# Optimization experiments

Hardware: AMD Instinct MI355X
Metric: run time of the kernel (lower is better)

Reference implementation:

```python
import jax, jax.numpy as jnp
import numpy as np

D_MODEL, HEADS, D_K = 512, 8, 64
MIN_SPREAD, MIN_RBF, MAX_RBF = 2.0, 0.001, 1.0
NEG_INF = float('-inf')


def setup_inputs() -> dict:
    key = jax.random.key(0)
    ks = jax.random.split(key, 12)
    B, N = 2, 2048
    xav = (6.0 / (D_K + D_MODEL)) ** 0.5
    unif = lambda k, shape: jax.random.uniform(k, shape, jnp.float32, -xav, xav)
    return {
        'q': jax.random.normal(ks[0], (B, N, D_MODEL), jnp.float32),
        'k': jax.random.normal(ks[1], (B, N, D_MODEL), jnp.float32),
        'v': jax.random.normal(ks[2], (B, N, D_MODEL), jnp.float32),
        'coords': jax.random.normal(ks[3], (B, N, 3), jnp.float32),
        'mask': jnp.zeros((B, N), dtype=bool),
        'spread_weights': jnp.zeros((HEADS,), jnp.float32),
        'beta_weights': jnp.zeros((HEADS,), jnp.float32),
        'q_proj': unif(ks[4], (HEADS, D_MODEL, D_K)),
        'k_proj': unif(ks[5], (HEADS, D_MODEL, D_K)),
        'v_proj': unif(ks[6], (HEADS, D_MODEL, D_K)),
        'q_bias': jnp.zeros((HEADS, D_K), jnp.float32),
        'k_bias': jnp.zeros((HEADS, D_K), jnp.float32),
        'v_bias': jnp.zeros((HEADS, D_K), jnp.float32),
        'w_out': jax.random.normal(ks[7], (D_MODEL, D_MODEL), jnp.float32) * (1.0 / D_MODEL ** 0.5),
    }


def reference(q, k, v, coords, mask, spread_weights, beta_weights,
              q_proj, k_proj, v_proj, q_bias, k_bias, v_bias, w_out):
    B, N, _ = q.shape
    # per-head projections: [B,H,N,dk]
    Q = jnp.einsum('bnd,hdk->bhnk', q, q_proj) + q_bias[None, :, None, :]
    K = jnp.einsum('bnd,hdk->bhnk', k, k_proj) + k_bias[None, :, None, :]
    V = jnp.einsum('bnd,hdk->bhnk', v, v_proj) + v_bias[None, :, None, :]
    # scaled dot-product scores [B,H,N,N]
    S = jnp.einsum('bhnk,bhmk->bhnm', Q, K) / (D_K ** 0.5)
    # squared pairwise distances [B,N,N] (D = sqrt(D2); RBF uses -D^2 = -D2)
    D2 = jnp.sum((coords[:, :, None, :] - coords[:, None, :, :]) ** 2, axis=-1)
    spreads = MIN_SPREAD + jnp.exp(spread_weights)  # [H]
    betas = jnp.exp(beta_weights)                   # [H]
    R = jnp.exp(-D2[:, None, :, :] / (2.0 * spreads[None, :, None, None] ** 2))
    R_norm = 2.0 * (R - MIN_RBF) / (MAX_RBF - MIN_RBF) - 1.0
    SR = S + jnp.abs(S) * betas[None, :, None, None] * R_norm
    SR = jnp.where(mask[:, None, None, :], NEG_INF, SR)  # eval mode: drop_p = 0
    P = jax.nn.softmax(SR, axis=-1)
    out = jnp.einsum('bhnm,bhmk->bhnk', P, V)  # [B,H,N,dk]
    # permute(0,2,3,1) -> [B,N,dk,H], reshape to [B,N,d_model]
    out = jnp.transpose(out, (0, 2, 3, 1)).reshape(B, N, D_MODEL)
    return out @ w_out.T
```

## Files before the change

### kernel.cpp

```cpp
#include <hip/hip_runtime.h>
#include <hip/hip_fp16.h>

typedef unsigned short u16;
typedef __attribute__((ext_vector_type(4))) float f32x4;
typedef __attribute__((ext_vector_type(8))) short s16x8;

#define NTHREADS 256
#define B_SZ 2
#define N_SZ 2048
#define H_SZ 8
#define DK 64
#define DM 512

static __device__ inline void mfma_f16(f32x4& acc, s16x8 a, s16x8 b) {
    asm volatile("v_mfma_f32_16x16x32_f16 %0, %1, %2, %0" : "+v"(acc) : "v"(a), "v"(b));
}

static __device__ inline u16 f16_rn(float f) {
    __half h = __float2half(f);
    return __half_as_ushort(h);
}

static __device__ inline s16x8 cvt8(const float4& a, const float4& b) {
    s16x8 r;
    r[0] = (short)f16_rn(a.x); r[1] = (short)f16_rn(a.y);
    r[2] = (short)f16_rn(a.z); r[3] = (short)f16_rn(a.w);
    r[4] = (short)f16_rn(b.x); r[5] = (short)f16_rn(b.y);
    r[6] = (short)f16_rn(b.z); r[7] = (short)f16_rn(b.w);
    return r;
}

__global__ void __launch_bounds__(NTHREADS) k_prep_proj(
    const float* __restrict__ qp, const float* __restrict__ kp,
    const float* __restrict__ vp, u16* __restrict__ Pt) {
    int ddt = blockIdx.x, h = blockIdx.y, z = blockIdx.z;
    const float* src = (z == 0 ? qp : (z == 1 ? kp : vp)) + (size_t)h * DM * DK;
    u16* dst = Pt + ((size_t)(z * H_SZ + h)) * DK * DM;
    __shared__ float lds[64 * 65];
    int t = threadIdx.x;
#pragma unroll
    for (int i = 0; i < 16; i++) {
        int idx = i * 256 + t;
        int rr = idx >> 6, cc = idx & 63;
        lds[cc * 65 + rr] = src[(size_t)(ddt * 64 + rr) * DK + cc];
    }
    __syncthreads();
#pragma unroll
    for (int i = 0; i < 16; i++) {
        int idx = i * 256 + t;
        int kk = idx >> 6, dd = idx & 63;
        dst[(size_t)kk * DM + ddt * 64 + dd] = f16_rn(lds[kk * 65 + dd]);
    }
}

__global__ void __launch_bounds__(NTHREADS) k_cvt_wout(
    const float* __restrict__ w, u16* __restrict__ wb) {
    int i = (blockIdx.x * 256 + threadIdx.x) * 4;
    float4 f = *(const float4*)(w + i);
    ushort4 r;
    r.x = f16_rn(f.x); r.y = f16_rn(f.y); r.z = f16_rn(f.z); r.w = f16_rn(f.w);
    *(ushort4*)(wb + i) = r;
}

__global__ void __launch_bounds__(NTHREADS) k_proj_gemm(
    const float* __restrict__ q, const float* __restrict__ k,
    const float* __restrict__ v, const u16* __restrict__ Pt,
    const float* __restrict__ qbias, const float* __restrict__ kbias,
    const float* __restrict__ vbias,
    u16* __restrict__ Qb, u16* __restrict__ Kb, u16* __restrict__ Vt) {
    int z = blockIdx.z;
    const float* A = z == 0 ? q : (z == 1 ? k : v);
    const float* bias = z == 0 ? qbias : (z == 1 ? kbias : vbias);
    const u16* Bw = Pt + (size_t)z * DM * DM;
    int m0 = blockIdx.x * 128, c0 = blockIdx.y * 64;
    int t = threadIdx.x, w = t >> 6, l = t & 63, g = l >> 4, cl = l & 15;
    __shared__ __align__(16) u16 a_lds[128 * 40];
    f32x4 acc[2][4] = {};
    int arow = t >> 1, ahalf = t & 1;
    const float* asrc = A + (size_t)(m0 + arow) * DM + ahalf * 16;
    u16* awr = &a_lds[arow * 40 + ahalf * 16];
    for (int ks = 0; ks < 16; ks++) {
        float4 f0 = *(const float4*)(asrc + ks * 32 + 0);
        float4 f1 = *(const float4*)(asrc + ks * 32 + 4);
        float4 f2 = *(const float4*)(asrc + ks * 32 + 8);
        float4 f3 = *(const float4*)(asrc + ks * 32 + 12);
        s16x8 bfrag[4];
#pragma unroll
        for (int st = 0; st < 4; st++) {
            int c = c0 + st * 16 + cl;
            bfrag[st] = *(const s16x8*)(Bw + (size_t)c * DM + ks * 32 + 8 * g);
        }
        __syncthreads();
        *(s16x8*)(awr) = cvt8(f0, f1);
        *(s16x8*)(awr + 8) = cvt8(f2, f3);
        __syncthreads();
#pragma unroll
        for (int rs = 0; rs < 2; rs++) {
            s16x8 afrag = *(const s16x8*)&a_lds[(w * 32 + rs * 16 + cl) * 40 + 8 * g];
#pragma unroll
            for (int st = 0; st < 4; st++) mfma_f16(acc[rs][st], afrag, bfrag[st]);
        }
    }
#pragma unroll
    for (int rs = 0; rs < 2; rs++) {
#pragma unroll
        for (int st = 0; st < 4; st++) {
            int c = c0 + st * 16 + cl;
            int h = c >> 6, kk = c & 63;
            float bv = bias[c];
#pragma unroll
            for (int r = 0; r < 4; r++) {
                int m = m0 + w * 32 + rs * 16 + 4 * g + r;
                int b = m >> 11, n = m & 2047;
                u16 o = f16_rn(acc[rs][st][r] + bv);
                if (z == 2) {
                    Vt[((size_t)((b * H_SZ + h) * 32 + (n >> 6))) * 4096 + kk * 64 + (n & 63)] = o;
                } else {
                    u16* dst = (z == 0) ? Qb : Kb;
                    dst[((size_t)(b * H_SZ + h) * N_SZ + n) * DK + kk] = o;
                }
            }
        }
    }
}

__global__ void __launch_bounds__(NTHREADS) k_attn(
    const u16* __restrict__ Qb, const u16* __restrict__ Kb,
    const u16* __restrict__ Vt, const float* __restrict__ coords,
    const unsigned char* __restrict__ maskp,
    const float* __restrict__ spread_w, const float* __restrict__ beta_w,
    float* __restrict__ Omat) {
    int qt = blockIdx.x, h = blockIdx.y, b = blockIdx.z;
    int n0 = qt * 64;
    int t = threadIdx.x, w = t >> 6, l = t & 63, g = l >> 4, cl = l & 15;
    int bh = b * H_SZ + h;
    __shared__ __align__(16) u16 k_lds[64 * 72];
    __shared__ __align__(16) u16 v_lds[64 * 72];
    __shared__ __align__(16) u16 p_lds[4][16 * 72];
    __shared__ float cj[64 * 4];
    __shared__ unsigned char msk[64];

    int qrow = n0 + w * 16 + cl;
    const u16* qp = Qb + ((size_t)bh * N_SZ + qrow) * DK;
    s16x8 qf0 = *(const s16x8*)(qp + 8 * g);
    s16x8 qf1 = *(const s16x8*)(qp + 32 + 8 * g);

    float qcx[4], qcy[4], qcz[4];
#pragma unroll
    for (int r = 0; r < 4; r++) {
        int row = n0 + w * 16 + 4 * g + r;
        const float* cp = coords + ((size_t)b * N_SZ + row) * 3;
        qcx[r] = cp[0]; qcy[r] = cp[1]; qcz[r] = cp[2];
    }
    float sigma = 2.0f + __expf(spread_w[h]);
    float ninv = -1.0f / (2.0f * sigma * sigma);
    float beta = __expf(beta_w[h]);

    float mrun[4] = {-1e30f, -1e30f, -1e30f, -1e30f};
    float lsum[4] = {0.f, 0.f, 0.f, 0.f};
    f32x4 oacc[4] = {};
    int srow = t >> 2, sq = t & 3;

    for (int jt = 0; jt < 32; jt++) {
        int j0 = jt * 64;
        __syncthreads();
        {
            const u16* ksrc = Kb + ((size_t)bh * N_SZ + j0 + srow) * DK + sq * 16;
            *(s16x8*)&k_lds[srow * 72 + sq * 16 + 0] = *(const s16x8*)(ksrc);
            *(s16x8*)&k_lds[srow * 72 + sq * 16 + 8] = *(const s16x8*)(ksrc + 8);
            const u16* vsrc = Vt + ((size_t)(bh * 32 + jt)) * 4096 + srow * 64 + sq * 16;
            *(s16x8*)&v_lds[srow * 72 + sq * 16 + 0] = *(const s16x8*)(vsrc);
            *(s16x8*)&v_lds[srow * 72 + sq * 16 + 8] = *(const s16x8*)(vsrc + 8);
            if (t < 64) {
                const float* cp = coords + ((size_t)b * N_SZ + j0 + t) * 3;
                cj[t * 4] = cp[0]; cj[t * 4 + 1] = cp[1]; cj[t * 4 + 2] = cp[2];
                msk[t] = maskp[b * N_SZ + j0 + t];
            }
        }
        __syncthreads();

        f32x4 s[4];
#pragma unroll
        for (int st = 0; st < 4; st++) {
            int jj = st * 16 + cl;
            s16x8 kf0 = *(const s16x8*)&k_lds[jj * 72 + 8 * g];
            s16x8 kf1 = *(const s16x8*)&k_lds[jj * 72 + 32 + 8 * g];
            f32x4 a = {};
            mfma_f16(a, qf0, kf0);
            mfma_f16(a, qf1, kf1);
            s[st] = a;
        }

        float sr[4][4];
#pragma unroll
        for (int st = 0; st < 4; st++) {
            int jj = st * 16 + cl;
            float cx = cj[jj * 4], cy = cj[jj * 4 + 1], cz = cj[jj * 4 + 2];
            bool mk = msk[jj] != 0;
#pragma unroll
            for (int r = 0; r < 4; r++) {
                float sv = s[st][r] * 0.125f;
                float dx = qcx[r] - cx, dy = qcy[r] - cy, dz = qcz[r] - cz;
                float d2 = dx * dx + dy * dy + dz * dz;
                float rb = __expf(d2 * ninv);
                float rn = fmaf(2.002002f, rb, -1.002002f);
                sv = fmaf(fabsf(sv) * beta, rn, sv);
                sr[st][r] = mk ? -1e30f : sv;
            }
        }
#pragma unroll
        for (int r = 0; r < 4; r++) {
            float tm = fmaxf(fmaxf(sr[0][r], sr[1][r]), fmaxf(sr[2][r], sr[3][r]));
            tm = fmaxf(tm, __shfl_xor(tm, 1));
            tm = fmaxf(tm, __shfl_xor(tm, 2));
            tm = fmaxf(tm, __shfl_xor(tm, 4));
            tm = fmaxf(tm, __shfl_xor(tm, 8));
            float mn = fmaxf(mrun[r], tm);
            float corr = __expf(mrun[r] - mn);
            mrun[r] = mn;
            lsum[r] *= corr;
#pragma unroll
            for (int dst = 0; dst < 4; dst++) oacc[dst][r] *= corr;
        }
#pragma unroll
        for (int st = 0; st < 4; st++) {
#pragma unroll
            for (int r = 0; r < 4; r++) {
                float p = __expf(sr[st][r] - mrun[r]);
                lsum[r] += p;
                p_lds[w][(4 * g + r) * 72 + st * 16 + cl] = f16_rn(p);
            }
        }
#pragma unroll
        for (int kstep = 0; kstep < 2; kstep++) {
            s16x8 pf = *(const s16x8*)&p_lds[w][cl * 72 + kstep * 32 + 8 * g];
#pragma unroll
            for (int dst = 0; dst < 4; dst++) {
                s16x8 vf = *(const s16x8*)&v_lds[(dst * 16 + cl) * 72 + kstep * 32 + 8 * g];
                mfma_f16(oacc[dst], pf, vf);
            }
        }
    }
#pragma unroll
    for (int r = 0; r < 4; r++) {
        float s = lsum[r];
        s += __shfl_xor(s, 1); s += __shfl_xor(s, 2);
        s += __shfl_xor(s, 4); s += __shfl_xor(s, 8);
        lsum[r] = 1.0f / s;
    }
#pragma unroll
    for (int dst = 0; dst < 4; dst++) {
#pragma unroll
        for (int r = 0; r < 4; r++) {
            int row = n0 + w * 16 + 4 * g + r;
            int col = (dst * 16 + cl) * 8 + h;
            Omat[((size_t)b * N_SZ + row) * DM + col] = oacc[dst][r] * lsum[r];
        }
    }
}

__global__ void __launch_bounds__(NTHREADS) k_out_gemm(
    const float* __restrict__ Omat, const u16* __restrict__ Wb,
    float* __restrict__ out) {
    int m0 = blockIdx.x * 128, c0 = blockIdx.y * 64;
    int t = threadIdx.x, w = t >> 6, l = t & 63, g = l >> 4, cl = l & 15;
    __shared__ __align__(16) u16 a_lds[128 * 40];
    f32x4 acc[2][4] = {};
    int arow = t >> 1, ahalf = t & 1;
    const float* asrc = Omat + (size_t)(m0 + arow) * DM + ahalf * 16;
    u16* awr = &a_lds[arow * 40 + ahalf * 16];
    for (int ks = 0; ks < 16; ks++) {
        float4 f0 = *(const float4*)(asrc + ks * 32 + 0);
        float4 f1 = *(const float4*)(asrc + ks * 32 + 4);
        float4 f2 = *(const float4*)(asrc + ks * 32 + 8);
        float4 f3 = *(const float4*)(asrc + ks * 32 + 12);
        s16x8 bfrag[4];
#pragma unroll
        for (int st = 0; st < 4; st++) {
            int c = c0 + st * 16 + cl;
            bfrag[st] = *(const s16x8*)(Wb + (size_t)c * DM + ks * 32 + 8 * g);
        }
        __syncthreads();
        *(s16x8*)(awr) = cvt8(f0, f1);
        *(s16x8*)(awr + 8) = cvt8(f2, f3);
        __syncthreads();
#pragma unroll
        for (int rs = 0; rs < 2; rs++) {
            s16x8 afrag = *(const s16x8*)&a_lds[(w * 32 + rs * 16 + cl) * 40 + 8 * g];
#pragma unroll
            for (int st = 0; st < 4; st++) mfma_f16(acc[rs][st], afrag, bfrag[st]);
        }
    }
#pragma unroll
    for (int rs = 0; rs < 2; rs++) {
#pragma unroll
        for (int st = 0; st < 4; st++) {
            int c = c0 + st * 16 + cl;
#pragma unroll
            for (int r = 0; r < 4; r++) {
                int m = m0 + w * 32 + rs * 16 + 4 * g + r;
                out[(size_t)m * DM + c] = acc[rs][st][r];
            }
        }
    }
}

extern "C" void kernel_launch(void* const* d_in, const int* in_sizes, int n_in,
                              void* d_out, int out_size, void* d_ws, size_t ws_size,
                              hipStream_t stream) {
    const float* q      = (const float*)d_in[0];
    const float* k      = (const float*)d_in[1];
    const float* v      = (const float*)d_in[2];
    const float* coords = (const float*)d_in[3];
    const unsigned char* mask = (const unsigned char*)d_in[4];
    const float* sw     = (const float*)d_in[5];
    const float* bw     = (const float*)d_in[6];
    const float* qp     = (const float*)d_in[7];
    const float* kp     = (const float*)d_in[8];
    const float* vp     = (const float*)d_in[9];
    const float* qbias  = (const float*)d_in[10];
    const float* kbias  = (const float*)d_in[11];
    const float* vbias  = (const float*)d_in[12];
    const float* wo     = (const float*)d_in[13];

    char* ws = (char*)d_ws;
    u16*   Pt   = (u16*)(ws);
    u16*   Wb   = (u16*)(ws + 1572864);
    u16*   Qb   = (u16*)(ws + 2097152);
    u16*   Kb   = (u16*)(ws + 6291456);
    u16*   Vt   = (u16*)(ws + 10485760);
    float* Omat = (float*)(ws + 14680064);

    k_prep_proj<<<dim3(8, 8, 3), NTHREADS, 0, stream>>>(qp, kp, vp, Pt);
    k_cvt_wout<<<dim3(256), NTHREADS, 0, stream>>>(wo, Wb);
    k_proj_gemm<<<dim3(32, 8, 3), NTHREADS, 0, stream>>>(q, k, v, Pt, qbias, kbias, vbias, Qb, Kb, Vt);
    k_attn<<<dim3(32, 8, 2), NTHREADS, 0, stream>>>(Qb, Kb, Vt, coords, mask, sw, bw, Omat);
    k_out_gemm<<<dim3(32, 8), NTHREADS, 0, stream>>>(Omat, Wb, (float*)d_out);
}
```

Before: 247.4 us.

## Split attention KV across two wave groups, swizzle LDS, precast activations to f16

Merges the prep kernels into one launch and pre-converts q/k/v to f16 so the projection GEMM can stage A tiles with direct global-to-LDS loads into XOR-swizzled shared memory using a larger K step. The attention kernel now runs 512 threads and splits the KV sequence between two wave halves, merging their softmax states at the end. It also folds the 1/sqrt(dk) scale into Q, skips the online-softmax rescale unless the max grows by more than a threshold, and remaps block ids. The output GEMM reads an f16 attention output with smaller tiles. These changes add extra memory traffic for the f16 copy of the inputs and a shared-memory merge step.

New measurement: 215.9 us. -12.7%, faster.

```diff
diff --git a/kernel.cpp b/kernel.cpp
--- a/kernel.cpp
+++ b/kernel.cpp
@@ -5,7 +5,6 @@
 typedef __attribute__((ext_vector_type(4))) float f32x4;
 typedef __attribute__((ext_vector_type(8))) short s16x8;
 
-#define NTHREADS 256
 #define B_SZ 2
 #define N_SZ 2048
 #define H_SZ 8
@@ -15,11 +14,7 @@
 static __device__ inline void mfma_f16(f32x4& acc, s16x8 a, s16x8 b) {
     asm volatile("v_mfma_f32_16x16x32_f16 %0, %1, %2, %0" : "+v"(acc) : "v"(a), "v"(b));
 }
-
-static __device__ inline u16 f16_rn(float f) {
-    __half h = __float2half(f);
-    return __half_as_ushort(h);
-}
+static __device__ inline u16 f16_rn(float f) { return __half_as_ushort(__float2half(f)); }
 
 static __device__ inline s16x8 cvt8(const float4& a, const float4& b) {
     s16x8 r;
@@ -30,77 +25,115 @@
     return r;
 }
 
-__global__ void __launch_bounds__(NTHREADS) k_prep_proj(
-    const float* __restrict__ qp, const float* __restrict__ kp,
-    const float* __restrict__ vp, u16* __restrict__ Pt) {
-    int ddt = blockIdx.x, h = blockIdx.y, z = blockIdx.z;
-    const float* src = (z == 0 ? qp : (z == 1 ? kp : vp)) + (size_t)h * DM * DK;
-    u16* dst = Pt + ((size_t)(z * H_SZ + h)) * DK * DM;
+static __device__ inline u16* swz(u16* base, int row, int byteoff) {
+    return (u16*)((char*)base + row * 128 + (byteoff ^ ((row & 7) << 4)));
+}
+static __device__ inline const u16* swzc(const u16* base, int row, int byteoff) {
+    return (const u16*)((const char*)base + row * 128 + (byteoff ^ ((row & 7) << 4)));
+}
+
+#if __has_builtin(__builtin_amdgcn_global_load_lds)
+#define HAS_GLL 1
+static __device__ inline void gll16(const u16* g, u16* l) {
+    __builtin_amdgcn_global_load_lds(
+        (const __attribute__((address_space(1))) unsigned int*)g,
+        (__attribute__((address_space(3))) unsigned int*)l, 16, 0, 0);
+}
+#endif
+
+static __device__ inline void stage16(const u16* gp, u16* lbase, int lane) {
+#ifdef HAS_GLL
+    gll16(gp, lbase);
+#else
+    *(s16x8*)(lbase + lane * 8) = *(const s16x8*)(gp);
+#endif
+}
+
+__global__ void __launch_bounds__(256) k_prep(
+    const float* __restrict__ q, const float* __restrict__ k,
+    const float* __restrict__ v, const float* __restrict__ qp,
+    const float* __restrict__ kp, const float* __restrict__ vp,
+    const float* __restrict__ wo,
+    u16* __restrict__ Pt, u16* __restrict__ Wb, u16* __restrict__ Af) {
+    int blk = blockIdx.x, t = threadIdx.x;
     __shared__ float lds[64 * 65];
-    int t = threadIdx.x;
-#pragma unroll
-    for (int i = 0; i < 16; i++) {
-        int idx = i * 256 + t;
-        int rr = idx >> 6, cc = idx & 63;
-        lds[cc * 65 + rr] = src[(size_t)(ddt * 64 + rr) * DK + cc];
-    }
-    __syncthreads();
-#pragma unroll
-    for (int i = 0; i < 16; i++) {
-        int idx = i * 256 + t;
-        int kk = idx >> 6, dd = idx & 63;
-        dst[(size_t)kk * DM + ddt * 64 + dd] = f16_rn(lds[kk * 65 + dd]);
-    }
-}
-
-__global__ void __launch_bounds__(NTHREADS) k_cvt_wout(
-    const float* __restrict__ w, u16* __restrict__ wb) {
-    int i = (blockIdx.x * 256 + threadIdx.x) * 4;
-    float4 f = *(const float4*)(w + i);
-    ushort4 r;
-    r.x = f16_rn(f.x); r.y = f16_rn(f.y); r.z = f16_rn(f.z); r.w = f16_rn(f.w);
-    *(ushort4*)(wb + i) = r;
-}
-
-__global__ void __launch_bounds__(NTHREADS) k_proj_gemm(
-    const float* __restrict__ q, const float* __restrict__ k,
-    const float* __restrict__ v, const u16* __restrict__ Pt,
+    if (blk < 192) {
+        int z = blk >> 6, rem = blk & 63, h = rem >> 3, ddt = rem & 7;
+        const float* src = (z == 0 ? qp : (z == 1 ? kp : vp)) + (size_t)h * DM * DK;
+        u16* dst = Pt + ((size_t)(z * H_SZ + h)) * DK * DM;
+#pragma unroll
+        for (int i = 0; i < 16; i++) {
+            int idx = i * 256 + t;
+            int rr = idx >> 6, cc = idx & 63;
+            lds[cc * 65 + rr] = src[(size_t)(ddt * 64 + rr) * DK + cc];
+        }
+        __syncthreads();
+#pragma unroll
+        for (int i = 0; i < 16; i++) {
+            int idx = i * 256 + t;
+            int kk = idx >> 6, dd = idx & 63;
+            dst[(size_t)kk * DM + ddt * 64 + dd] = f16_rn(lds[kk * 65 + dd]);
+        }
+    } else if (blk < 448) {
+        int i = (blk - 192) * 1024 + t * 4;
+        float4 f = *(const float4*)(wo + i);
+        ushort4 r;
+        r.x = f16_rn(f.x); r.y = f16_rn(f.y); r.z = f16_rn(f.z); r.w = f16_rn(f.w);
+        *(ushort4*)(Wb + i) = r;
+    } else {
+        size_t base = (size_t)(blk - 448) * 2048 + (size_t)t * 8;
+        int z = (int)(base >> 21);
+        size_t off = base & 2097151;
+        const float* s = (z == 0 ? q : (z == 1 ? k : v)) + off;
+        float4 f0 = *(const float4*)(s);
+        float4 f1 = *(const float4*)(s + 4);
+        *(s16x8*)(Af + base) = cvt8(f0, f1);
+    }
+}
+
+__global__ void __launch_bounds__(256) k_proj_gemm(
+    const u16* __restrict__ Af, const u16* __restrict__ Pt,
     const float* __restrict__ qbias, const float* __restrict__ kbias,
     const float* __restrict__ vbias,
     u16* __restrict__ Qb, u16* __restrict__ Kb, u16* __restrict__ Vt) {
     int z = blockIdx.z;
-    const float* A = z == 0 ? q : (z == 1 ? k : v);
+    const u16* A = Af + (size_t)z * (4096 * 512);
     const float* bias = z == 0 ? qbias : (z == 1 ? kbias : vbias);
-    const u16* Bw = Pt + (size_t)z * DM * DM;
+    const u16* Bw = Pt + (size_t)z * (512 * 512);
     int m0 = blockIdx.x * 128, c0 = blockIdx.y * 64;
-    int t = threadIdx.x, w = t >> 6, l = t & 63, g = l >> 4, cl = l & 15;
-    __shared__ __align__(16) u16 a_lds[128 * 40];
+    int t = threadIdx.x, w = t >> 6, l = t & 63, g = (l >> 4), cl = l & 15;
+    __shared__ __align__(16) u16 a_lds[128 * 64];
     f32x4 acc[2][4] = {};
-    int arow = t >> 1, ahalf = t & 1;
-    const float* asrc = A + (size_t)(m0 + arow) * DM + ahalf * 16;
-    u16* awr = &a_lds[arow * 40 + ahalf * 16];
-    for (int ks = 0; ks < 16; ks++) {
-        float4 f0 = *(const float4*)(asrc + ks * 32 + 0);
-        float4 f1 = *(const float4*)(asrc + ks * 32 + 4);
-        float4 f2 = *(const float4*)(asrc + ks * 32 + 8);
-        float4 f3 = *(const float4*)(asrc + ks * 32 + 12);
-        s16x8 bfrag[4];
+    int srow_b = w * 8 + (l >> 3), schk = l & 7;
+    for (int ks = 0; ks < 8; ks++) {
+        __syncthreads();
+#pragma unroll
+        for (int cc = 0; cc < 4; cc++) {
+            int row = cc * 32 + srow_b;
+            const u16* gp = A + (size_t)(m0 + row) * 512 + ks * 64 + ((schk ^ (row & 7)) << 3);
+            stage16(gp, a_lds + cc * 2048 + w * 512, l);
+        }
+        s16x8 bfrag[4][2];
 #pragma unroll
         for (int st = 0; st < 4; st++) {
             int c = c0 + st * 16 + cl;
-            bfrag[st] = *(const s16x8*)(Bw + (size_t)c * DM + ks * 32 + 8 * g);
-        }
-        __syncthreads();
-        *(s16x8*)(awr) = cvt8(f0, f1);
-        *(s16x8*)(awr + 8) = cvt8(f2, f3);
+#pragma unroll
+            for (int kk = 0; kk < 2; kk++)
+                bfrag[st][kk] = *(const s16x8*)(Bw + (size_t)c * 512 + ks * 64 + kk * 32 + 8 * g);
+        }
         __syncthreads();
 #pragma unroll
         for (int rs = 0; rs < 2; rs++) {
-            s16x8 afrag = *(const s16x8*)&a_lds[(w * 32 + rs * 16 + cl) * 40 + 8 * g];
-#pragma unroll
-            for (int st = 0; st < 4; st++) mfma_f16(acc[rs][st], afrag, bfrag[st]);
-        }
-    }
+            int row = w * 32 + rs * 16 + cl;
+#pragma unroll
+            for (int kk = 0; kk < 2; kk++) {
+                s16x8 afrag = *(const s16x8*)swzc(a_lds, row, kk * 64 + 16 * g);
+#pragma unroll
+                for (int st = 0; st < 4; st++) mfma_f16(acc[rs][st], afrag, bfrag[st][kk]);
+            }
+        }
+    }
+    float sc = (z == 0) ? 0.125f : 1.0f;
 #pragma unroll
     for (int rs = 0; rs < 2; rs++) {
 #pragma unroll
@@ -112,7 +145,7 @@
             for (int r = 0; r < 4; r++) {
                 int m = m0 + w * 32 + rs * 16 + 4 * g + r;
                 int b = m >> 11, n = m & 2047;
-                u16 o = f16_rn(acc[rs][st][r] + bv);
+                u16 o = f16_rn((acc[rs][st][r] + bv) * sc);
                 if (z == 2) {
                     Vt[((size_t)((b * H_SZ + h) * 32 + (n >> 6))) * 4096 + kk * 64 + (n & 63)] = o;
                 } else {
@@ -124,23 +157,26 @@
     }
 }
 
-__global__ void __launch_bounds__(NTHREADS) k_attn(
+__global__ void __launch_bounds__(512, 4) k_attn(
     const u16* __restrict__ Qb, const u16* __restrict__ Kb,
     const u16* __restrict__ Vt, const float* __restrict__ coords,
     const unsigned char* __restrict__ maskp,
     const float* __restrict__ spread_w, const float* __restrict__ beta_w,
-    float* __restrict__ Omat) {
-    int qt = blockIdx.x, h = blockIdx.y, b = blockIdx.z;
+    u16* __restrict__ Om) {
+    int bid = blockIdx.x;
+    int wid = (bid & 7) * 64 + (bid >> 3);
+    int qt = wid & 31, bh = wid >> 5;
+    int h = bh & 7, b = bh >> 3;
     int n0 = qt * 64;
-    int t = threadIdx.x, w = t >> 6, l = t & 63, g = l >> 4, cl = l & 15;
-    int bh = b * H_SZ + h;
-    __shared__ __align__(16) u16 k_lds[64 * 72];
-    __shared__ __align__(16) u16 v_lds[64 * 72];
-    __shared__ __align__(16) u16 p_lds[4][16 * 72];
-    __shared__ float cj[64 * 4];
-    __shared__ unsigned char msk[64];
-
-    int qrow = n0 + w * 16 + cl;
+    int t = threadIdx.x, w = t >> 6, l = t & 63, g = (l >> 4), cl = l & 15;
+    int wq = w & 3, half = w >> 2;
+    __shared__ __align__(16) u16 kbuf[2][4096];
+    __shared__ __align__(16) u16 vbuf[2][4096];
+    __shared__ __align__(16) u16 pbuf[8][1024];
+    __shared__ float cjs[2][64][4];
+    __shared__ unsigned char msks[2][64];
+
+    int qrow = n0 + wq * 16 + cl;
     const u16* qp = Qb + ((size_t)bh * N_SZ + qrow) * DK;
     s16x8 qf0 = *(const s16x8*)(qp + 8 * g);
     s16x8 qf1 = *(const s16x8*)(qp + 32 + 8 * g);
@@ -148,7 +184,7 @@
     float qcx[4], qcy[4], qcz[4];
 #pragma unroll
     for (int r = 0; r < 4; r++) {
-        int row = n0 + w * 16 + 4 * g + r;
+        int row = n0 + wq * 16 + 4 * g + r;
         const float* cp = coords + ((size_t)b * N_SZ + row) * 3;
         qcx[r] = cp[0]; qcy[r] = cp[1]; qcz[r] = cp[2];
     }
@@ -159,22 +195,26 @@
     float mrun[4] = {-1e30f, -1e30f, -1e30f, -1e30f};
     float lsum[4] = {0.f, 0.f, 0.f, 0.f};
     f32x4 oacc[4] = {};
-    int srow = t >> 2, sq = t & 3;
-
-    for (int jt = 0; jt < 32; jt++) {
-        int j0 = jt * 64;
+    int sid = t & 255, shalf = t >> 8, srow = sid >> 2, sq = sid & 3;
+    const u16* kbase = Kb + (size_t)bh * N_SZ * DK;
+    const u16* vbase = Vt + (size_t)bh * 32 * 4096;
+
+    for (int it = 0; it < 16; it++) {
+        int jts = it * 2 + shalf, j0s = jts * 64;
         __syncthreads();
         {
-            const u16* ksrc = Kb + ((size_t)bh * N_SZ + j0 + srow) * DK + sq * 16;
-            *(s16x8*)&k_lds[srow * 72 + sq * 16 + 0] = *(const s16x8*)(ksrc);
-            *(s16x8*)&k_lds[srow * 72 + sq * 16 + 8] = *(const s16x8*)(ksrc + 8);
-            const u16* vsrc = Vt + ((size_t)(bh * 32 + jt)) * 4096 + srow * 64 + sq * 16;
-            *(s16x8*)&v_lds[srow * 72 + sq * 16 + 0] = *(const s16x8*)(vsrc);
-            *(s16x8*)&v_lds[srow * 72 + sq * 16 + 8] = *(const s16x8*)(vsrc + 8);
-            if (t < 64) {
-                const float* cp = coords + ((size_t)b * N_SZ + j0 + t) * 3;
-                cj[t * 4] = cp[0]; cj[t * 4 + 1] = cp[1]; cj[t * 4 + 2] = cp[2];
-                msk[t] = maskp[b * N_SZ + j0 + t];
+            const u16* ksrc = kbase + (size_t)(j0s + srow) * 64 + sq * 16;
+            *(s16x8*)swz(kbuf[shalf], srow, sq * 32)      = *(const s16x8*)(ksrc);
+            *(s16x8*)swz(kbuf[shalf], srow, sq * 32 + 16) = *(const s16x8*)(ksrc + 8);
+            const u16* vsrc = vbase + (size_t)jts * 4096 + srow * 64 + sq * 16;
+            *(s16x8*)swz(vbuf[shalf], srow, sq * 32)      = *(const s16x8*)(vsrc);
+            *(s16x8*)swz(vbuf[shalf], srow, sq * 32 + 16) = *(const s16x8*)(vsrc + 8);
+            if (sid < 64) {
+                const float* cp = coords + ((size_t)b * N_SZ + j0s + sid) * 3;
+                cjs[shalf][sid][0] = cp[0];
+                cjs[shalf][sid][1] = cp[1];
+                cjs[shalf][sid][2] = cp[2];
+                msks[shalf][sid] = maskp[b * N_SZ + j0s + sid];
             }
         }
         __syncthreads();
@@ -183,31 +223,31 @@
 #pragma unroll
         for (int st = 0; st < 4; st++) {
             int jj = st * 16 + cl;
-            s16x8 kf0 = *(const s16x8*)&k_lds[jj * 72 + 8 * g];
-            s16x8 kf1 = *(const s16x8*)&k_lds[jj * 72 + 32 + 8 * g];
+            s16x8 kf0 = *(const s16x8*)swzc(kbuf[half], jj, 16 * g);
+            s16x8 kf1 = *(const s16x8*)swzc(kbuf[half], jj, 64 + 16 * g);
             f32x4 a = {};
             mfma_f16(a, qf0, kf0);
             mfma_f16(a, qf1, kf1);
             s[st] = a;
         }
-
         float sr[4][4];
 #pragma unroll
         for (int st = 0; st < 4; st++) {
             int jj = st * 16 + cl;
-            float cx = cj[jj * 4], cy = cj[jj * 4 + 1], cz = cj[jj * 4 + 2];
-            bool mk = msk[jj] != 0;
+            float cx = cjs[half][jj][0], cy = cjs[half][jj][1], cz = cjs[half][jj][2];
+            bool mk = msks[half][jj] != 0;
 #pragma unroll
             for (int r = 0; r < 4; r++) {
-                float sv = s[st][r] * 0.125f;
+                float sv = s[st][r];
                 float dx = qcx[r] - cx, dy = qcy[r] - cy, dz = qcz[r] - cz;
-                float d2 = dx * dx + dy * dy + dz * dz;
+                float d2 = fmaf(dx, dx, fmaf(dy, dy, dz * dz));
                 float rb = __expf(d2 * ninv);
                 float rn = fmaf(2.002002f, rb, -1.002002f);
                 sv = fmaf(fabsf(sv) * beta, rn, sv);
                 sr[st][r] = mk ? -1e30f : sv;
             }
         }
+        float tmx[4]; int need = 0;
 #pragma unroll
         for (int r = 0; r < 4; r++) {
             float tm = fmaxf(fmaxf(sr[0][r], sr[1][r]), fmaxf(sr[2][r], sr[3][r]));
@@ -215,12 +255,19 @@
             tm = fmaxf(tm, __shfl_xor(tm, 2));
             tm = fmaxf(tm, __shfl_xor(tm, 4));
             tm = fmaxf(tm, __shfl_xor(tm, 8));
-            float mn = fmaxf(mrun[r], tm);
-            float corr = __expf(mrun[r] - mn);
-            mrun[r] = mn;
-            lsum[r] *= corr;
-#pragma unroll
-            for (int dst = 0; dst < 4; dst++) oacc[dst][r] *= corr;
+            tmx[r] = tm;
+            if (tm > mrun[r] + 8.0f) need = 1;
+        }
+        if (__any(need)) {
+#pragma unroll
+            for (int r = 0; r < 4; r++) {
+                float mn = fmaxf(mrun[r], tmx[r]);
+                float corr = __expf(mrun[r] - mn);
+                mrun[r] = mn;
+                lsum[r] *= corr;
+#pragma unroll
+                for (int dst = 0; dst < 4; dst++) oacc[dst][r] *= corr;
+            }
         }
 #pragma unroll
         for (int st = 0; st < 4; st++) {
@@ -228,15 +275,16 @@
             for (int r = 0; r < 4; r++) {
                 float p = __expf(sr[st][r] - mrun[r]);
                 lsum[r] += p;
-                p_lds[w][(4 * g + r) * 72 + st * 16 + cl] = f16_rn(p);
+                int row = 4 * g + r;
+                *swz(pbuf[w], row, (st * 16 + cl) * 2) = f16_rn(p);
             }
         }
 #pragma unroll
         for (int kstep = 0; kstep < 2; kstep++) {
-            s16x8 pf = *(const s16x8*)&p_lds[w][cl * 72 + kstep * 32 + 8 * g];
+            s16x8 pf = *(const s16x8*)swzc(pbuf[w], cl, kstep * 64 + 16 * g);
 #pragma unroll
             for (int dst = 0; dst < 4; dst++) {
-                s16x8 vf = *(const s16x8*)&v_lds[(dst * 16 + cl) * 72 + kstep * 32 + 8 * g];
+                s16x8 vf = *(const s16x8*)swzc(vbuf[half], dst * 16 + cl, kstep * 64 + 16 * g);
                 mfma_f16(oacc[dst], pf, vf);
             }
         }
@@ -246,61 +294,83 @@
         float s = lsum[r];
         s += __shfl_xor(s, 1); s += __shfl_xor(s, 2);
         s += __shfl_xor(s, 4); s += __shfl_xor(s, 8);
-        lsum[r] = 1.0f / s;
-    }
-#pragma unroll
-    for (int dst = 0; dst < 4; dst++) {
+        lsum[r] = s;
+    }
+    __syncthreads();
+    float* scrO = (float*)(&kbuf[0][0]);
+    float* scrM = (float*)(&vbuf[0][0]);
+    if (half == 1) {
 #pragma unroll
         for (int r = 0; r < 4; r++) {
-            int row = n0 + w * 16 + 4 * g + r;
-            int col = (dst * 16 + cl) * 8 + h;
-            Omat[((size_t)b * N_SZ + row) * DM + col] = oacc[dst][r] * lsum[r];
-        }
-    }
-}
-
-__global__ void __launch_bounds__(NTHREADS) k_out_gemm(
-    const float* __restrict__ Omat, const u16* __restrict__ Wb,
+            int rr = 4 * g + r;
+#pragma unroll
+            for (int dst = 0; dst < 4; dst++)
+                scrO[wq * 1024 + rr * 64 + dst * 16 + cl] = oacc[dst][r];
+            if (cl == 0) {
+                scrM[wq * 32 + rr] = mrun[r];
+                scrM[wq * 32 + 16 + rr] = lsum[r];
+            }
+        }
+    }
+    __syncthreads();
+    if (half == 0) {
+#pragma unroll
+        for (int r = 0; r < 4; r++) {
+            int rr = 4 * g + r;
+            float mu = scrM[wq * 32 + rr], lu = scrM[wq * 32 + 16 + rr];
+            float M = fmaxf(mrun[r], mu);
+            float pa = __expf(mrun[r] - M), pb = __expf(mu - M);
+            float inv = 1.0f / (pa * lsum[r] + pb * lu);
+            int row = n0 + wq * 16 + rr;
+#pragma unroll
+            for (int dst = 0; dst < 4; dst++) {
+                float o = (pa * oacc[dst][r] + pb * scrO[wq * 1024 + rr * 64 + dst * 16 + cl]) * inv;
+                Om[((size_t)b * N_SZ + row) * DM + (dst * 16 + cl) * 8 + h] = f16_rn(o);
+            }
+        }
+    }
+}
+
+__global__ void __launch_bounds__(256) k_out_gemm(
+    const u16* __restrict__ Om, const u16* __restrict__ Wb,
     float* __restrict__ out) {
-    int m0 = blockIdx.x * 128, c0 = blockIdx.y * 64;
-    int t = threadIdx.x, w = t >> 6, l = t & 63, g = l >> 4, cl = l & 15;
-    __shared__ __align__(16) u16 a_lds[128 * 40];
-    f32x4 acc[2][4] = {};
-    int arow = t >> 1, ahalf = t & 1;
-    const float* asrc = Omat + (size_t)(m0 + arow) * DM + ahalf * 16;
-    u16* awr = &a_lds[arow * 40 + ahalf * 16];
-    for (int ks = 0; ks < 16; ks++) {
-        float4 f0 = *(const float4*)(asrc + ks * 32 + 0);
-        float4 f1 = *(const float4*)(asrc + ks * 32 + 4);
-        float4 f2 = *(const float4*)(asrc + ks * 32 + 8);
-        float4 f3 = *(const float4*)(asrc + ks * 32 + 12);
-        s16x8 bfrag[4];
+    int m0 = blockIdx.x * 64, c0 = blockIdx.y * 64;
+    int t = threadIdx.x, w = t >> 6, l = t & 63, g = (l >> 4), cl = l & 15;
+    __shared__ __align__(16) u16 a_lds[64 * 64];
+    f32x4 acc[4] = {};
+    int srow_b = w * 8 + (l >> 3), schk = l & 7;
+    for (int ks = 0; ks < 8; ks++) {
+        __syncthreads();
+#pragma unroll
+        for (int cc = 0; cc < 2; cc++) {
+            int row = cc * 32 + srow_b;
+            const u16* gp = Om + (size_t)(m0 + row) * 512 + ks * 64 + ((schk ^ (row & 7)) << 3);
+            stage16(gp, a_lds + cc * 2048 + w * 512, l);
+        }
+        s16x8 bfrag[4][2];
 #pragma unroll
         for (int st = 0; st < 4; st++) {
             int c = c0 + st * 16 + cl;
-            bfrag[st] = *(const s16x8*)(Wb + (size_t)c * DM + ks * 32 + 8 * g);
-        }
-        __syncthreads();
-        *(s16x8*)(awr) = cvt8(f0, f1);
-        *(s16x8*)(awr + 8) = cvt8(f2, f3);
-        __syncthreads();
-#pragma unroll
-        for (int rs = 0; rs < 2; rs++) {
-            s16x8 afrag = *(const s16x8*)&a_lds[(w * 32 + rs * 16 + cl) * 40 + 8 * g];
-#pragma unroll
-            for (int st = 0; st < 4; st++) mfma_f16(acc[rs][st], afrag, bfrag[st]);
-        }
-    }
-#pragma unroll
-    for (int rs = 0; rs < 2; rs++) {
-#pragma unroll
-        for (int st = 0; st < 4; st++) {
-            int c = c0 + st * 16 + cl;
-#pragma unroll
-            for (int r = 0; r < 4; r++) {
-                int m = m0 + w * 32 + rs * 16 + 4 * g + r;
-                out[(size_t)m * DM + c] = acc[rs][st][r];
-            }
+#pragma unroll
+            for (int kk = 0; kk < 2; kk++)
+                bfrag[st][kk] = *(const s16x8*)(Wb + (size_t)c * 512 + ks * 64 + kk * 32 + 8 * g);
+        }
+        __syncthreads();
+        int row = w * 16 + cl;
+#pragma unroll
+        for (int kk = 0; kk < 2; kk++) {
+            s16x8 afrag = *(const s16x8*)swzc(a_lds, row, kk * 64 + 16 * g);
+#pragma unroll
+            for (int st = 0; st < 4; st++) mfma_f16(acc[st], afrag, bfrag[st][kk]);
+        }
+    }
+#pragma unroll
+    for (int st = 0; st < 4; st++) {
+        int c = c0 + st * 16 + cl;
+#pragma unroll
+        for (int r = 0; r < 4; r++) {
+            int m = m0 + w * 16 + 4 * g + r;
+            out[(size_t)m * 512 + c] = acc[st][r];
         }
     }
 }
@@ -324,16 +394,16 @@
     const float* wo     = (const float*)d_in[13];
 
     char* ws = (char*)d_ws;
-    u16*   Pt   = (u16*)(ws);
-    u16*   Wb   = (u16*)(ws + 1572864);
-    u16*   Qb   = (u16*)(ws + 2097152);
-    u16*   Kb   = (u16*)(ws + 6291456);
-    u16*   Vt   = (u16*)(ws + 10485760);
-    float* Omat = (float*)(ws + 14680064);
-
-    k_prep_proj<<<dim3(8, 8, 3), NTHREADS, 0, stream>>>(qp, kp, vp, Pt);
-    k_cvt_wout<<<dim3(256), NTHREADS, 0, stream>>>(wo, Wb);
-    k_proj_gemm<<<dim3(32, 8, 3), NTHREADS, 0, stream>>>(q, k, v, Pt, qbias, kbias, vbias, Qb, Kb, Vt);
-    k_attn<<<dim3(32, 8, 2), NTHREADS, 0, stream>>>(Qb, Kb, Vt, coords, mask, sw, bw, Omat);
-    k_out_gemm<<<dim3(32, 8), NTHREADS, 0, stream>>>(Omat, Wb, (float*)d_out);
-}
+    u16* Pt = (u16*)(ws);
+    u16* Wb = (u16*)(ws + 1572864);
+    u16* Af = (u16*)(ws + 2097152);
+    u16* Qb = (u16*)(ws + 14680064);
+    u16* Kb = (u16*)(ws + 18874368);
+    u16* Vt = (u16*)(ws + 23068672);
+    u16* Om = (u16*)(ws + 27262976);
+
+    k_prep<<<dim3(3520), 256, 0, stream>>>(q, k, v, qp, kp, vp, wo, Pt, Wb, Af);
+    k_proj_gemm<<<dim3(32, 8, 3), 256, 0, stream>>>(Af, Pt, qbias, kbias, vbias, Qb, Kb, Vt);
+    k_attn<<<dim3(512), 512, 0, stream>>>(Qb, Kb, Vt, coords, mask, sw, bw, Om);
+    k_out_gemm<<<dim3(64, 8), 256, 0, stream>>>(Om, Wb, (float*)d_out);
+}
```
